# Performance work log

Measured on AMD Instinct MI355X. Metric: run time of the kernel, lower is better.

The kernel has to match this reference:

```python
import jax, jax.numpy as jnp
import numpy as np

RMS_EPS = 1.1920928955078125e-07  # torch.finfo(float32).eps, nn.RMSNorm default when eps=None


def setup_inputs() -> dict:
    key = jax.random.key(0)
    ks = jax.random.split(key, 7)
    B, T, C, Wh, E, K = 8, 4096, 256, 1024, 8, 2
    return {
        "x": jax.random.normal(ks[0], (B, T, C), dtype=jnp.float32),
        "rms_weight": jnp.ones((C,), dtype=jnp.float32),
        "W1": jax.random.normal(ks[1], (E, C, Wh), dtype=jnp.float32),
        "b1": jax.random.normal(ks[2], (E, Wh), dtype=jnp.float32),
        "W2": jax.random.normal(ks[3], (E, Wh, C), dtype=jnp.float32),
        "b2": jax.random.normal(ks[4], (E, C), dtype=jnp.float32),
        "expert_ids": jax.random.randint(ks[5], (B, T, K), 0, E, dtype=jnp.int64),
    }


def reference(x, rms_weight, W1, b1, W2, b2, expert_ids):
    # RMSNorm over last dim (torch nn.RMSNorm, eps = float32 eps)
    xn = x * jax.lax.rsqrt(jnp.mean(x * x, axis=-1, keepdims=True) + RMS_EPS) * rms_weight
    # Per-expert 2-layer MLP. The torch code gathers per-token weight copies then bmm's;
    # mathematically identical (and far cheaper in memory) is: run every expert densely,
    # then gather the K selected expert outputs per token.
    h = jax.nn.gelu(jnp.einsum("btc,ecw->btew", xn, W1) + b1, approximate=False)  # [B,T,E,Wh]
    y = jnp.einsum("btew,ewc->btec", h, W2) + b2  # [B,T,E,C]
    # gather selected experts: [B,T,K,C]; dropout p is 0.0 (eval) -> identity
    out = jnp.take_along_axis(y, expert_ids[..., None], axis=2)
    return out
```

## Files before the change

kernel.cpp:

```cpp
#include <hip/hip_runtime.h>
#include <cstdint>

typedef unsigned short ushort_t;
typedef __bf16 bf16x8 __attribute__((ext_vector_type(8)));
typedef ushort_t u16x8 __attribute__((ext_vector_type(8)));
typedef float f32x4 __attribute__((ext_vector_type(4)));
typedef uint32_t u32x4 __attribute__((ext_vector_type(4)));

#define RMS_EPS 1.1920928955078125e-07f

__device__ __forceinline__ ushort_t f2bf(float f) {
  uint32_t u = __builtin_bit_cast(uint32_t, f);
  u += 0x7fffu + ((u >> 16) & 1u);
  return (ushort_t)(u >> 16);
}

__device__ __forceinline__ void g2l16(const ushort_t* g, ushort_t* l) {
  __builtin_amdgcn_global_load_lds(
      (const __attribute__((address_space(1))) uint32_t*)g,
      (__attribute__((address_space(3))) uint32_t*)l, 16, 0, 0);
}

__global__ void rmsnorm_cast(const float* __restrict__ x, const float* __restrict__ w,
                             ushort_t* __restrict__ xn) {
  int token = blockIdx.x * 4 + (threadIdx.x >> 6);
  int lane = threadIdx.x & 63;
  const float4* row = reinterpret_cast<const float4*>(x + (size_t)token * 256);
  float4 v = row[lane];
  float s = v.x * v.x + v.y * v.y + v.z * v.z + v.w * v.w;
#pragma unroll
  for (int off = 1; off < 64; off <<= 1) s += __shfl_xor(s, off);
  float inv = rsqrtf(s * (1.0f / 256.0f) + RMS_EPS);
  const float4* wr = reinterpret_cast<const float4*>(w);
  float4 wv = wr[lane];
  ushort4 o;
  o.x = f2bf(v.x * inv * wv.x);
  o.y = f2bf(v.y * inv * wv.y);
  o.z = f2bf(v.z * inv * wv.z);
  o.w = f2bf(v.w * inv * wv.w);
  *reinterpret_cast<ushort4*>(xn + (size_t)token * 256 + lane * 4) = o;
}

__global__ __launch_bounds__(256) void pack_w(const float* __restrict__ W1,
                                              const float* __restrict__ W2,
                                              ushort_t* __restrict__ w1f,
                                              ushort_t* __restrict__ w2f) {
  __shared__ ushort_t tile[64][130];
  int b = blockIdx.x;
  int isW2 = b >= 256;
  const float* src; ushort_t* dst; int e, kt, wt, rs;
  if (!isW2) { e = b >> 5; kt = (b >> 3) & 3; wt = b & 7; src = W1; dst = w1f; rs = 1024; }
  else { b -= 256; e = b >> 5; kt = (b >> 1) & 15; wt = b & 1; src = W2; dst = w2f; rs = 256; }
  int k0 = kt * 64, c0 = wt * 128;
  const float* sb = src + ((size_t)e << 18) + (size_t)k0 * rs + c0;
  int t = threadIdx.x;
#pragma unroll
  for (int i = 0; i < 8; ++i) {
    int f = i * 1024 + t * 4;
    int r = f >> 7, c = f & 127;
    float4 v = *reinterpret_cast<const float4*>(sb + (size_t)r * rs + c);
    ushort2 lo, hi;
    lo.x = f2bf(v.x); lo.y = f2bf(v.y); hi.x = f2bf(v.z); hi.y = f2bf(v.w);
    *reinterpret_cast<ushort2*>(&tile[r][c]) = lo;
    *reinterpret_cast<ushort2*>(&tile[r][c + 2]) = hi;
  }
  __syncthreads();
  int lane = t & 63, l16 = lane & 15, quad = lane >> 4;
#pragma unroll
  for (int p = 0; p < 4; ++p) {
    int u = p * 256 + t;
    int kk2 = (u >> 9) & 1;
    int rr = kk2 * 32 + quad * 8;
    u16x8 o;
    size_t U;
    if (!isW2) {
      int nt = (u >> 6) & 1, chL = (u >> 7) & 3;
      int cc = chL * 32 + nt * 16 + l16;
#pragma unroll
      for (int j = 0; j < 8; ++j) o[j] = tile[rr + j][cc];
      U = ((size_t)e * 32768) + (size_t)(wt * 4 + chL) * 1024 + (kt * 2 + kk2) * 128 + nt * 64 + lane;
    } else {
      int ntL = (u >> 6) & 7;
      int cc = ntL * 16 + l16;
#pragma unroll
      for (int j = 0; j < 8; ++j) o[j] = tile[rr + j][cc];
      U = ((size_t)e * 32768) + (size_t)(kt * 2 + kk2) * 1024 + (wt * 8 + ntL) * 64 + lane;
    }
    *reinterpret_cast<u16x8*>(dst + U * 8) = o;
  }
}

__global__ void route_pairs(const int* __restrict__ eids, int* __restrict__ cnt,
                            int* __restrict__ lists) {
  __shared__ int lcnt[8], lbase[8];
  int tid = threadIdx.x;
  if (tid < 8) lcnt[tid] = 0;
  __syncthreads();
  int p = blockIdx.x * 256 + tid;
  int e = eids[p];
  int lpos = atomicAdd(&lcnt[e], 1);
  __syncthreads();
  if (tid < 8) lbase[tid] = atomicAdd(&cnt[tid], lcnt[tid]);
  __syncthreads();
  lists[e * 65536 + lbase[e] + lpos] = p;
}

__global__ __launch_bounds__(256, 2) void moe_mlp(
    const ushort_t* __restrict__ xn,
    const ushort_t* __restrict__ w1f,
    const ushort_t* __restrict__ w2f,
    const float* __restrict__ b1,
    const float* __restrict__ b2,
    const int* __restrict__ cnt,
    const int* __restrict__ lists,
    float* __restrict__ out)
{
  __shared__ __align__(16) ushort_t w1b[2][8192];
  __shared__ __align__(16) ushort_t w2b[2][8192];
  __shared__ __align__(16) ushort_t hlds[4][32][40];
  __shared__ int prs[128];

  int flat = blockIdx.x;
  int e = -1, tile = 0, accum = 0, n_e = 0;
#pragma unroll
  for (int i = 0; i < 8; ++i) {
    int c = cnt[i];
    int t = (c + 127) >> 7;
    if (e < 0 && flat < accum + t) { e = i; tile = flat - accum; n_e = c; }
    accum += t;
  }
  if (e < 0) return;
  int start = tile * 128;

  int tid = threadIdx.x;
  if (tid < 128) {
    int idx = start + tid;
    prs[tid] = (idx < n_e) ? lists[e * 65536 + idx] : lists[e * 65536];
  }

  const ushort_t* w1e = w1f + ((size_t)e << 18);
  const ushort_t* w2e = w2f + ((size_t)e << 18);
  int wave = tid >> 6, lane = tid & 63, l16 = lane & 15, quad = lane >> 4;

#pragma unroll
  for (int j = 0; j < 4; ++j) {
    int p = j * 4 + wave;
    g2l16(w1e + p * 512 + lane * 8, &w1b[0][p * 512]);
    g2l16(w2e + p * 512 + lane * 8, &w2b[0][p * 512]);
  }
  __syncthreads();

  bf16x8 afr[2][8];
#pragma unroll
  for (int mt = 0; mt < 2; ++mt) {
    int tok = prs[wave * 32 + mt * 16 + l16] >> 1;
    const u32x4* arow = reinterpret_cast<const u32x4*>(xn + (size_t)tok * 256);
#pragma unroll
    for (int kk = 0; kk < 8; ++kk)
      afr[mt][kk] = __builtin_bit_cast(bf16x8, arow[kk * 4 + quad]);
  }

  f32x4 acc[2][16];
#pragma unroll
  for (int mt = 0; mt < 2; ++mt)
#pragma unroll
    for (int ct = 0; ct < 16; ++ct) acc[mt][ct] = (f32x4){0.f, 0.f, 0.f, 0.f};

  const float* b1e = b1 + e * 1024;
  ushort_t* hl = &hlds[wave][0][0];

  for (int ch = 0; ch < 32; ++ch) {
    int cur = ch & 1;
    __syncthreads();
    if (ch + 1 < 32) {
      const ushort_t* n1 = w1e + (ch + 1) * 8192;
      const ushort_t* n2 = w2e + (ch + 1) * 8192;
#pragma unroll
      for (int j = 0; j < 4; ++j) {
        int p = j * 4 + wave;
        g2l16(n1 + p * 512 + lane * 8, &w1b[cur ^ 1][p * 512]);
        g2l16(n2 + p * 512 + lane * 8, &w2b[cur ^ 1][p * 512]);
      }
    }
    const ushort_t* l1 = w1b[cur];
    const ushort_t* l2 = w2b[cur];
    int w0 = ch * 32;
    float bias0 = b1e[w0 + l16];
    float bias1 = b1e[w0 + 16 + l16];

    f32x4 h00 = (f32x4){0.f, 0.f, 0.f, 0.f};
    f32x4 h01 = (f32x4){0.f, 0.f, 0.f, 0.f};
    f32x4 h10 = (f32x4){0.f, 0.f, 0.f, 0.f};
    f32x4 h11 = (f32x4){0.f, 0.f, 0.f, 0.f};
#pragma unroll
    for (int kk = 0; kk < 8; ++kk) {
      bf16x8 bA = *reinterpret_cast<const bf16x8*>(l1 + ((kk * 2 + 0) * 64 + lane) * 8);
      h00 = __builtin_amdgcn_mfma_f32_16x16x32_bf16(afr[0][kk], bA, h00, 0, 0, 0);
      h01 = __builtin_amdgcn_mfma_f32_16x16x32_bf16(afr[1][kk], bA, h01, 0, 0, 0);
    }
#pragma unroll
    for (int kk = 0; kk < 8; ++kk) {
      bf16x8 bB = *reinterpret_cast<const bf16x8*>(l1 + ((kk * 2 + 1) * 64 + lane) * 8);
      h10 = __builtin_amdgcn_mfma_f32_16x16x32_bf16(afr[0][kk], bB, h10, 0, 0, 0);
      h11 = __builtin_amdgcn_mfma_f32_16x16x32_bf16(afr[1][kk], bB, h11, 0, 0, 0);
    }
#pragma unroll
    for (int r = 0; r < 4; ++r) {
      {
        float v = h00[r] + bias0;
        float v2 = v * v;
        float u_ = (0.044715f * v2) * v + v;
        float tq = __expf(-1.5957691216057308f * u_);
        float g = v * __builtin_amdgcn_rcpf(1.0f + tq);
        hl[(quad * 4 + r) * 40 + l16] = f2bf(g);
      }
      {
        float v = h01[r] + bias0;
        float v2 = v * v;
        float u_ = (0.044715f * v2) * v + v;
        float tq = __expf(-1.5957691216057308f * u_);
        float g = v * __builtin_amdgcn_rcpf(1.0f + tq);
        hl[(16 + quad * 4 + r) * 40 + l16] = f2bf(g);
      }
      {
        float v = h10[r] + bias1;
        float v2 = v * v;
        float u_ = (0.044715f * v2) * v + v;
        float tq = __expf(-1.5957691216057308f * u_);
        float g = v * __builtin_amdgcn_rcpf(1.0f + tq);
        hl[(quad * 4 + r) * 40 + 16 + l16] = f2bf(g);
      }
      {
        float v = h11[r] + bias1;
        float v2 = v * v;
        float u_ = (0.044715f * v2) * v + v;
        float tq = __expf(-1.5957691216057308f * u_);
        float g = v * __builtin_amdgcn_rcpf(1.0f + tq);
        hl[(16 + quad * 4 + r) * 40 + 16 + l16] = f2bf(g);
      }
    }
    bf16x8 a2_0 = *reinterpret_cast<const bf16x8*>(hl + l16 * 40 + quad * 8);
    bf16x8 a2_1 = *reinterpret_cast<const bf16x8*>(hl + (16 + l16) * 40 + quad * 8);

#pragma unroll
    for (int ct = 0; ct < 16; ++ct) {
      bf16x8 b = *reinterpret_cast<const bf16x8*>(l2 + (ct * 64 + lane) * 8);
      acc[0][ct] = __builtin_amdgcn_mfma_f32_16x16x32_bf16(a2_0, b, acc[0][ct], 0, 0, 0);
      acc[1][ct] = __builtin_amdgcn_mfma_f32_16x16x32_bf16(a2_1, b, acc[1][ct], 0, 0, 0);
    }
  }

  const float* b2e = b2 + e * 256;
  float bl[16];
#pragma unroll
  for (int ct = 0; ct < 16; ++ct) bl[ct] = b2e[ct * 16 + l16];
#pragma unroll
  for (int mt = 0; mt < 2; ++mt) {
#pragma unroll
    for (int r = 0; r < 4; ++r) {
      int m = wave * 32 + mt * 16 + quad * 4 + r;
      if (start + m < n_e) {
        float* orow = out + (size_t)prs[m] * 256;
#pragma unroll
        for (int ct = 0; ct < 16; ++ct)
          orow[ct * 16 + l16] = acc[mt][ct][r] + bl[ct];
      }
    }
  }
}

extern "C" void kernel_launch(void* const* d_in, const int* in_sizes, int n_in,
                              void* d_out, int out_size, void* d_ws, size_t ws_size,
                              hipStream_t stream) {
  const float* x  = (const float*)d_in[0];
  const float* rw = (const float*)d_in[1];
  const float* W1 = (const float*)d_in[2];
  const float* b1 = (const float*)d_in[3];
  const float* W2 = (const float*)d_in[4];
  const float* b2 = (const float*)d_in[5];
  const int* eids = (const int*)d_in[6];
  float* out = (float*)d_out;

  char* ws = (char*)d_ws;
  ushort_t* xn  = (ushort_t*)(ws);
  ushort_t* w1f = (ushort_t*)(ws + 16777216);
  ushort_t* w2f = (ushort_t*)(ws + 20971520);
  int* cnt      = (int*)(ws + 25165824);
  int* lists    = (int*)(ws + 25166080);

  hipMemsetAsync(cnt, 0, 8 * sizeof(int), stream);
  rmsnorm_cast<<<8192, 256, 0, stream>>>(x, rw, xn);
  pack_w<<<512, 256, 0, stream>>>(W1, W2, w1f, w2f);
  route_pairs<<<256, 256, 0, stream>>>(eids, cnt, lists);
  moe_mlp<<<519, 256, 0, stream>>>(xn, w1f, w2f, b1, b2, cnt, lists, out);
}
```

Measured before the change: 253.3 us.

## Single-buffer W2 in LDS and split GELU to cut LDS and register use

The W2 chunk buffer in shared memory drops from double to single buffering, which frees LDS. The next W2 chunk is now loaded after a barrier that follows the second GEMM, so that load is no longer overlapped with a whole iteration. The first-layer accumulators are split into two sequential halves, each followed immediately by its GELU, which lowers live registers, and waves_per_eu(2) is added as an occupancy hint. The risk is exposed W2 load latency and an extra barrier in every iteration.

New measurement: 291.0 us. 1.15x slower.

```diff
diff --git a/kernel.cpp b/kernel.cpp
--- a/kernel.cpp
+++ b/kernel.cpp
@@ -105,7 +105,9 @@
   lists[e * 65536 + lbase[e] + lpos] = p;
 }
 
-__global__ __launch_bounds__(256, 2) void moe_mlp(
+__global__ __launch_bounds__(256, 2)
+__attribute__((amdgpu_waves_per_eu(2)))
+void moe_mlp(
     const ushort_t* __restrict__ xn,
     const ushort_t* __restrict__ w1f,
     const ushort_t* __restrict__ w2f,
@@ -116,7 +118,7 @@
     float* __restrict__ out)
 {
   __shared__ __align__(16) ushort_t w1b[2][8192];
-  __shared__ __align__(16) ushort_t w2b[2][8192];
+  __shared__ __align__(16) ushort_t w2b[8192];
   __shared__ __align__(16) ushort_t hlds[4][32][40];
   __shared__ int prs[128];
 
@@ -146,7 +148,7 @@
   for (int j = 0; j < 4; ++j) {
     int p = j * 4 + wave;
     g2l16(w1e + p * 512 + lane * 8, &w1b[0][p * 512]);
-    g2l16(w2e + p * 512 + lane * 8, &w2b[0][p * 512]);
+    g2l16(w2e + p * 512 + lane * 8, &w2b[p * 512]);
   }
   __syncthreads();
 
@@ -171,72 +173,61 @@
 
   for (int ch = 0; ch < 32; ++ch) {
     int cur = ch & 1;
-    __syncthreads();
+    if (ch) __syncthreads();
     if (ch + 1 < 32) {
       const ushort_t* n1 = w1e + (ch + 1) * 8192;
-      const ushort_t* n2 = w2e + (ch + 1) * 8192;
 #pragma unroll
       for (int j = 0; j < 4; ++j) {
         int p = j * 4 + wave;
         g2l16(n1 + p * 512 + lane * 8, &w1b[cur ^ 1][p * 512]);
-        g2l16(n2 + p * 512 + lane * 8, &w2b[cur ^ 1][p * 512]);
       }
     }
     const ushort_t* l1 = w1b[cur];
-    const ushort_t* l2 = w2b[cur];
     int w0 = ch * 32;
-    float bias0 = b1e[w0 + l16];
-    float bias1 = b1e[w0 + 16 + l16];
-
-    f32x4 h00 = (f32x4){0.f, 0.f, 0.f, 0.f};
-    f32x4 h01 = (f32x4){0.f, 0.f, 0.f, 0.f};
-    f32x4 h10 = (f32x4){0.f, 0.f, 0.f, 0.f};
-    f32x4 h11 = (f32x4){0.f, 0.f, 0.f, 0.f};
+
+    f32x4 ha, hb;
+    ha = (f32x4){0.f, 0.f, 0.f, 0.f};
+    hb = (f32x4){0.f, 0.f, 0.f, 0.f};
 #pragma unroll
     for (int kk = 0; kk < 8; ++kk) {
       bf16x8 bA = *reinterpret_cast<const bf16x8*>(l1 + ((kk * 2 + 0) * 64 + lane) * 8);
-      h00 = __builtin_amdgcn_mfma_f32_16x16x32_bf16(afr[0][kk], bA, h00, 0, 0, 0);
-      h01 = __builtin_amdgcn_mfma_f32_16x16x32_bf16(afr[1][kk], bA, h01, 0, 0, 0);
-    }
+      ha = __builtin_amdgcn_mfma_f32_16x16x32_bf16(afr[0][kk], bA, ha, 0, 0, 0);
+      hb = __builtin_amdgcn_mfma_f32_16x16x32_bf16(afr[1][kk], bA, hb, 0, 0, 0);
+    }
+    {
+      float bias0 = b1e[w0 + l16];
+#pragma unroll
+      for (int r = 0; r < 4; ++r) {
+        float v = ha[r] + bias0;
+        float u_ = (0.044715f * v * v) * v + v;
+        float tq = __expf(-1.5957691216057308f * u_);
+        hl[(quad * 4 + r) * 40 + l16] = f2bf(v * __builtin_amdgcn_rcpf(1.0f + tq));
+        float v2 = hb[r] + bias0;
+        float u2 = (0.044715f * v2 * v2) * v2 + v2;
+        float tq2 = __expf(-1.5957691216057308f * u2);
+        hl[(16 + quad * 4 + r) * 40 + l16] = f2bf(v2 * __builtin_amdgcn_rcpf(1.0f + tq2));
+      }
+    }
+    ha = (f32x4){0.f, 0.f, 0.f, 0.f};
+    hb = (f32x4){0.f, 0.f, 0.f, 0.f};
 #pragma unroll
     for (int kk = 0; kk < 8; ++kk) {
       bf16x8 bB = *reinterpret_cast<const bf16x8*>(l1 + ((kk * 2 + 1) * 64 + lane) * 8);
-      h10 = __builtin_amdgcn_mfma_f32_16x16x32_bf16(afr[0][kk], bB, h10, 0, 0, 0);
-      h11 = __builtin_amdgcn_mfma_f32_16x16x32_bf16(afr[1][kk], bB, h11, 0, 0, 0);
-    }
-#pragma unroll
-    for (int r = 0; r < 4; ++r) {
-      {
-        float v = h00[r] + bias0;
-        float v2 = v * v;
-        float u_ = (0.044715f * v2) * v + v;
+      ha = __builtin_amdgcn_mfma_f32_16x16x32_bf16(afr[0][kk], bB, ha, 0, 0, 0);
+      hb = __builtin_amdgcn_mfma_f32_16x16x32_bf16(afr[1][kk], bB, hb, 0, 0, 0);
+    }
+    {
+      float bias1 = b1e[w0 + 16 + l16];
+#pragma unroll
+      for (int r = 0; r < 4; ++r) {
+        float v = ha[r] + bias1;
+        float u_ = (0.044715f * v * v) * v + v;
         float tq = __expf(-1.5957691216057308f * u_);
-        float g = v * __builtin_amdgcn_rcpf(1.0f + tq);
-        hl[(quad * 4 + r) * 40 + l16] = f2bf(g);
-      }
-      {
-        float v = h01[r] + bias0;
-        float v2 = v * v;
-        float u_ = (0.044715f * v2) * v + v;
-        float tq = __expf(-1.5957691216057308f * u_);
-        float g = v * __builtin_amdgcn_rcpf(1.0f + tq);
-        hl[(16 + quad * 4 + r) * 40 + l16] = f2bf(g);
-      }
-      {
-        float v = h10[r] + bias1;
-        float v2 = v * v;
-        float u_ = (0.044715f * v2) * v + v;
-        float tq = __expf(-1.5957691216057308f * u_);
-        float g = v * __builtin_amdgcn_rcpf(1.0f + tq);
-        hl[(quad * 4 + r) * 40 + 16 + l16] = f2bf(g);
-      }
-      {
-        float v = h11[r] + bias1;
-        float v2 = v * v;
-        float u_ = (0.044715f * v2) * v + v;
-        float tq = __expf(-1.5957691216057308f * u_);
-        float g = v * __builtin_amdgcn_rcpf(1.0f + tq);
-        hl[(16 + quad * 4 + r) * 40 + 16 + l16] = f2bf(g);
+        hl[(quad * 4 + r) * 40 + 16 + l16] = f2bf(v * __builtin_amdgcn_rcpf(1.0f + tq));
+        float v2 = hb[r] + bias1;
+        float u2 = (0.044715f * v2 * v2) * v2 + v2;
+        float tq2 = __expf(-1.5957691216057308f * u2);
+        hl[(16 + quad * 4 + r) * 40 + 16 + l16] = f2bf(v2 * __builtin_amdgcn_rcpf(1.0f + tq2));
       }
     }
     bf16x8 a2_0 = *reinterpret_cast<const bf16x8*>(hl + l16 * 40 + quad * 8);
@@ -244,9 +235,18 @@
 
 #pragma unroll
     for (int ct = 0; ct < 16; ++ct) {
-      bf16x8 b = *reinterpret_cast<const bf16x8*>(l2 + (ct * 64 + lane) * 8);
+      bf16x8 b = *reinterpret_cast<const bf16x8*>(w2b + (ct * 64 + lane) * 8);
       acc[0][ct] = __builtin_amdgcn_mfma_f32_16x16x32_bf16(a2_0, b, acc[0][ct], 0, 0, 0);
       acc[1][ct] = __builtin_amdgcn_mfma_f32_16x16x32_bf16(a2_1, b, acc[1][ct], 0, 0, 0);
+    }
+    __syncthreads();
+    if (ch + 1 < 32) {
+      const ushort_t* n2 = w2e + (ch + 1) * 8192;
+#pragma unroll
+      for (int j = 0; j < 4; ++j) {
+        int p = j * 4 + wave;
+        g2l16(n2 + p * 512 + lane * 8, &w2b[p * 512]);
+      }
     }
   }
 
```
